# Performance work log

Hardware: AMD Instinct MI355X
Metric: run time of the kernel (lower is better)

## Reference

```python
import jax, jax.numpy as jnp
import numpy as np

DIM = 256
EPS = 1e-5

def setup_inputs() -> dict:
    key = jax.random.key(0)
    ks = jax.random.split(key, 10)
    B, S, D = 8, 4096, DIM
    sc = 1.0 / np.sqrt(D)
    return {
        "supervised_embedding": jax.random.normal(ks[0], (B, S, D), jnp.float32),
        "transformer_embedding": jax.random.normal(ks[1], (B, S, D), jnp.float32),
        "Wq": jax.random.normal(ks[2], (D, D), jnp.float32) * sc,
        "bq": jnp.zeros((D,), jnp.float32),
        "Wk": jax.random.normal(ks[3], (D, D), jnp.float32) * sc,
        "bk": jnp.zeros((D,), jnp.float32),
        "Wv": jax.random.normal(ks[4], (D, D), jnp.float32) * sc,
        "bv": jnp.zeros((D,), jnp.float32),
        "gamma": jnp.ones((D,), jnp.float32),
        "beta": jnp.zeros((D,), jnp.float32),
    }

def _layernorm(x, gamma, beta):
    mu = jnp.mean(x, axis=-1, keepdims=True)
    var = jnp.mean(jnp.square(x - mu), axis=-1, keepdims=True)
    return (x - mu) * jax.lax.rsqrt(var + EPS) * gamma + beta

def reference(supervised_embedding, transformer_embedding, Wq, bq, Wk, bk, Wv, bv, gamma, beta):
    # torch Linear: y = x @ W.T + b
    q = transformer_embedding @ Wq.T + bq          # [B,S,D]
    k = supervised_embedding @ Wk.T + bk           # [B,S,D]
    v = supervised_embedding @ Wv.T + bv           # [B,S,D]
    scale = 1.0 / jnp.sqrt(jnp.asarray(q.shape[-1], q.dtype))
    scores = jnp.einsum('bqd,bkd->bqk', q, k) * scale  # [B,S,S]
    w = jax.nn.softmax(scores, axis=-1)
    combined = jnp.einsum('bqk,bkd->bqd', w, v)    # [B,S,D]
    out = _layernorm(combined + transformer_embedding, gamma, beta)
    return jnp.squeeze(out, axis=1) if out.shape[1] == 1 else out
```

## Files before the change

kernel.cpp:

```cpp
#include <hip/hip_runtime.h>
#include <hip/hip_bf16.h>

typedef short s16x8 __attribute__((ext_vector_type(8)));
typedef unsigned short u16x4 __attribute__((ext_vector_type(4)));
typedef float f32x4 __attribute__((ext_vector_type(4)));
typedef unsigned short u16;

#define DEV static __device__ __forceinline__

#if __has_builtin(__builtin_amdgcn_exp2f)
#define EXP2F(x) __builtin_amdgcn_exp2f(x)
#else
#define EXP2F(x) exp2f(x)
#endif

constexpr int D    = 256;
constexpr int SEQ  = 4096;
constexpr int NB   = 8;
constexpr int NTOK = NB * SEQ;
constexpr size_t N_EMB = (size_t)NTOK * D;
constexpr size_t N_W   = (size_t)D * D;
constexpr float SM_C = 0.09016844005556021f;
constexpr float SMAX = 128.0f;

DEV u16 f2bf(float f){ unsigned v; __builtin_memcpy(&v,&f,4); v += 0x7fffu + ((v>>16)&1u); return (u16)(v>>16); }

DEV float rsum16(float v){
  v += __shfl_xor(v,1); v += __shfl_xor(v,2);
  v += __shfl_xor(v,4); v += __shfl_xor(v,8);
  return v;
}

DEV void gl2lds16(const u16* g, void* lds){
  __builtin_amdgcn_global_load_lds(
      (const __attribute__((address_space(1))) void*)g,
      (__attribute__((address_space(3))) void*)lds, 16, 0, 0);
}
DEV void lgkm_barrier(){
  __builtin_amdgcn_s_waitcnt(0xC07F);
  __builtin_amdgcn_s_barrier();
}

DEV s16x8 cvt8(const float* p){
  f32x4 u = *(const f32x4*)p;
  f32x4 w = *(const f32x4*)(p + 4);
  s16x8 t;
#pragma unroll
  for (int j = 0; j < 4; j++){ t[j] = (short)f2bf(u[j]); t[j+4] = (short)f2bf(w[j]); }
  return t;
}

__global__ __launch_bounds__(256)
void cvt_w(const float* __restrict__ Wq, const float* __restrict__ Wk,
           const float* __restrict__ Wv, u16* __restrict__ dst)
{
  size_t i = ((size_t)blockIdx.x*256 + threadIdx.x) * 4;
  const float* s = (i < N_W) ? (Wq + i) : (i < 2*N_W) ? (Wk + i - N_W) : (Wv + i - 2*N_W);
  f32x4 v = *(const f32x4*)s;
  u16x4 o;
#pragma unroll
  for (int j = 0; j < 4; j++) o[j] = f2bf(v[j]);
  *(u16x4*)(dst + i) = o;
}

__global__ __launch_bounds__(256, 2)
void qkv_proj(const float* __restrict__ TE, const float* __restrict__ SE,
              const u16* __restrict__ Wqb, const float* __restrict__ bq,
              const u16* __restrict__ Wkb, const float* __restrict__ bk,
              const u16* __restrict__ Wvb, const float* __restrict__ bv,
              u16* __restrict__ Qb, u16* __restrict__ Kb, u16* __restrict__ Vt)
{
  const int mode = blockIdx.y;
  const int t0   = blockIdx.x * 64;
  const int lane = threadIdx.x & 63;
  const int wv   = threadIdx.x >> 6;
  const int li   = lane & 15, grp = lane >> 4;

  const float* X    = (mode == 0) ? TE  : SE;
  const u16*   W    = (mode == 0) ? Wqb : (mode == 1) ? Wkb : Wvb;
  const float* bias = (mode == 0) ? bq  : (mode == 1) ? bk  : bv;

  if (mode < 2) {
    u16* Y = (mode == 0) ? Qb : Kb;
    const float* xrow = X + (size_t)(t0 + 16*wv + li) * D + grp*8;
    s16x8 a[8];
#pragma unroll
    for (int ks = 0; ks < 8; ks++) a[ks] = cvt8(xrow + ks*32);
    f32x4 acc[16];
#pragma unroll
    for (int i = 0; i < 16; i++) acc[i] = (f32x4){0.f,0.f,0.f,0.f};
#pragma unroll
    for (int nt = 0; nt < 16; nt++) {
      const u16* wrow = W + (size_t)(16*nt + li) * D + grp*8;
#pragma unroll
      for (int ks = 0; ks < 8; ks++) {
        s16x8 bf = *(const s16x8*)(wrow + ks*32);
        acc[nt] = __builtin_amdgcn_mfma_f32_16x16x32_bf16(a[ks], bf, acc[nt], 0,0,0);
      }
    }
#pragma unroll
    for (int nt = 0; nt < 16; nt++) {
      int col = li + 16*nt;
      float bb = bias[col];
#pragma unroll
      for (int r = 0; r < 4; r++) {
        int row = t0 + 16*wv + grp*4 + r;
        Y[(size_t)row*D + col] = f2bf(acc[nt][r] + bb);
      }
    }
  } else {
    f32x4 acc[16];
#pragma unroll
    for (int i = 0; i < 16; i++) acc[i] = (f32x4){0.f,0.f,0.f,0.f};
#pragma unroll
    for (int ks = 0; ks < 8; ks++) {
      s16x8 a[4], bb[4];
#pragma unroll
      for (int mt = 0; mt < 4; mt++)
        a[mt] = *(const s16x8*)(W + (size_t)(64*wv + 16*mt + li) * D + ks*32 + grp*8);
#pragma unroll
      for (int nt = 0; nt < 4; nt++)
        bb[nt] = cvt8(X + (size_t)(t0 + 16*nt + li) * D + ks*32 + grp*8);
#pragma unroll
      for (int mt = 0; mt < 4; mt++)
#pragma unroll
        for (int nt = 0; nt < 4; nt++)
          acc[mt*4+nt] = __builtin_amdgcn_mfma_f32_16x16x32_bf16(a[mt], bb[nt], acc[mt*4+nt], 0,0,0);
    }
    const int b = t0 >> 12, s0 = t0 & (SEQ - 1);
#pragma unroll
    for (int mt = 0; mt < 4; mt++) {
#pragma unroll
      for (int r = 0; r < 4; r++) {
        int o = 64*wv + 16*mt + grp*4 + r;
        float bb = bias[o];
        u16* yrow = Vt + ((size_t)b * D + o) * SEQ + s0;
#pragma unroll
        for (int nt = 0; nt < 4; nt++)
          yrow[16*nt + li] = f2bf(acc[mt*4+nt][r] + bb);
      }
    }
  }
}

constexpr int KB0   = 0;
constexpr int KB1   = 16384;
constexpr int P_OFF = 32768;
constexpr int PSTR  = 36;
constexpr int L_OFF = 37376;
constexpr int G_OFF = 37632;
constexpr int BE_OFF= 38656;
constexpr int LDS_SZ= 39680;
constexpr int NIT   = SEQ / 32;

__global__ __launch_bounds__(256, 2)
void attn_ln(const u16* __restrict__ Qb, const u16* __restrict__ Kb,
             const u16* __restrict__ Vt, const float* __restrict__ TE,
             const float* __restrict__ gamma, const float* __restrict__ beta,
             float* __restrict__ out)
{
  __shared__ __align__(16) char smem[LDS_SZ];
  const int tid  = threadIdx.x;
  const int lane = tid & 63, wv = tid >> 6;
  const int li   = lane & 15, grp = lane >> 4;
  const int b  = blockIdx.x & 7;
  const int q0 = (blockIdx.x >> 3) * 64;

  float* gam = (float*)(smem + G_OFF);
  float* bet = (float*)(smem + BE_OFF);
  gam[tid] = gamma[tid];
  bet[tid] = beta[tid];

  const u16* Kbase = Kb + (size_t)b * SEQ * D;
  const u16* Vbase = Vt + (size_t)b * D * SEQ;

  const u16* qrow = Qb + ((size_t)b*SEQ + q0 + 16*wv + li)*D + grp*8;
  s16x8 qf[8];
#pragma unroll
  for (int ks = 0; ks < 8; ks++) qf[ks] = *(const s16x8*)(qrow + ks*32);

  int soff[4];
#pragma unroll
  for (int c = 0; c < 4; c++) {
    int u = wv*4 + c;
    int r = 2*u + (lane >> 5);
    soff[c] = r*256 + (((lane & 31) ^ (r & 7)) * 8);
  }
  int voff[4];
#pragma unroll
  for (int nt = 0; nt < 4; nt++) voff[nt] = (64*wv + 16*nt + li)*SEQ + grp*8;

#pragma unroll
  for (int c = 0; c < 4; c++)
    gl2lds16(Kbase + soff[c], smem + KB0 + (wv*4 + c)*1024);

  f32x4 oacc[16];
#pragma unroll
  for (int i = 0; i < 16; i++) oacc[i] = (f32x4){0.f,0.f,0.f,0.f};
  float l_r[4] = {0.f,0.f,0.f,0.f};

  u16* Pl = (u16*)(smem + P_OFF);

  for (int it = 0; it < NIT; it++) {
    const int k0 = it * 32;
    __syncthreads();

    {
      const u16* Kt = Kbase + (size_t)((it+1 < NIT) ? (k0+32) : k0) * D;
      char* kbn = smem + ((it & 1) ? KB0 : KB1);
#pragma unroll
      for (int c = 0; c < 4; c++)
        gl2lds16(Kt + soff[c], kbn + (wv*4 + c)*1024);
    }
    s16x8 vf[4];
#pragma unroll
    for (int nt = 0; nt < 4; nt++)
      vf[nt] = *(const s16x8*)(Vbase + voff[nt] + k0);

    const char* kb = smem + ((it & 1) ? KB1 : KB0);
    f32x4 sa0 = {0.f,0.f,0.f,0.f}, sa1 = {0.f,0.f,0.f,0.f};
    {
      const int r0 = li, r1 = li + 16;
      const char* kp0 = kb + r0*512;
      const char* kp1 = kb + r1*512;
#pragma unroll
      for (int ks = 0; ks < 8; ks++) {
        s16x8 k0f = *(const s16x8*)(kp0 + 16*((4*ks + grp) ^ (r0 & 7)));
        sa0 = __builtin_amdgcn_mfma_f32_16x16x32_bf16(qf[ks], k0f, sa0, 0,0,0);
        s16x8 k1f = *(const s16x8*)(kp1 + 16*((4*ks + grp) ^ (r1 & 7)));
        sa1 = __builtin_amdgcn_mfma_f32_16x16x32_bf16(qf[ks], k1f, sa1, 0,0,0);
      }
    }

#pragma unroll
    for (int r = 0; r < 4; r++) {
      float p0 = EXP2F((sa0[r] - SMAX) * SM_C);
      float p1 = EXP2F((sa1[r] - SMAX) * SM_C);
      l_r[r] += p0 + p1;
      int row = 16*wv + grp*4 + r;
      Pl[row*PSTR + li]      = f2bf(p0);
      Pl[row*PSTR + li + 16] = f2bf(p1);
    }
    lgkm_barrier();

#pragma unroll
    for (int mt = 0; mt < 4; mt++) {
      s16x8 pf = *(const s16x8*)(smem + P_OFF + ((16*mt + li)*PSTR + grp*8)*2);
#pragma unroll
      for (int nt = 0; nt < 4; nt++)
        oacc[mt*4+nt] = __builtin_amdgcn_mfma_f32_16x16x32_bf16(pf, vf[nt], oacc[mt*4+nt], 0,0,0);
    }
  }

  float* l_lds = (float*)(smem + L_OFF);
  {
#pragma unroll
    for (int r = 0; r < 4; r++) {
      float lt = rsum16(l_r[r]);
      if (li == 0) l_lds[16*wv + grp*4 + r] = lt;
    }
  }
  __syncthreads();

  const float* Tg = TE + ((size_t)b*SEQ + q0) * D;
  float s1[4][4], s2[4][4];
#pragma unroll
  for (int mt = 0; mt < 4; mt++) {
#pragma unroll
    for (int r = 0; r < 4; r++) {
      int row = 16*mt + grp*4 + r;
      float linv = 1.0f / l_lds[row];
      float ps = 0.f, pq = 0.f;
#pragma unroll
      for (int nt = 0; nt < 4; nt++) {
        int d_ = 64*wv + 16*nt + li;
        float x = oacc[mt*4+nt][r] * linv + Tg[(size_t)row*D + d_];
        oacc[mt*4+nt][r] = x;
        ps += x; pq += x * x;
      }
      s1[mt][r] = rsum16(ps);
      s2[mt][r] = rsum16(pq);
    }
  }
  float* part1 = (float*)(smem + P_OFF);
  float* part2 = (float*)(smem + P_OFF + 1024);
  if (li == 0) {
#pragma unroll
    for (int mt = 0; mt < 4; mt++)
#pragma unroll
      for (int r = 0; r < 4; r++) {
        int row = 16*mt + grp*4 + r;
        part1[row*4 + wv] = s1[mt][r];
        part2[row*4 + wv] = s2[mt][r];
      }
  }
  __syncthreads();
#pragma unroll
  for (int mt = 0; mt < 4; mt++) {
#pragma unroll
    for (int r = 0; r < 4; r++) {
      int row = 16*mt + grp*4 + r;
      float su = part1[row*4+0] + part1[row*4+1] + part1[row*4+2] + part1[row*4+3];
      float sq = part2[row*4+0] + part2[row*4+1] + part2[row*4+2] + part2[row*4+3];
      float mu  = su * (1.0f/256.0f);
      float var = sq * (1.0f/256.0f) - mu*mu;
      float rstd = rsqrtf(var + 1e-5f);
      float* orow = out + ((size_t)b*SEQ + q0 + row) * D;
#pragma unroll
      for (int nt = 0; nt < 4; nt++) {
        int d_ = 64*wv + 16*nt + li;
        orow[d_] = (oacc[mt*4+nt][r] - mu) * rstd * gam[d_] + bet[d_];
      }
    }
  }
}

extern "C" void kernel_launch(void* const* d_in, const int* in_sizes, int n_in,
                              void* d_out, int out_size, void* d_ws, size_t ws_size,
                              hipStream_t stream)
{
  (void)in_sizes; (void)n_in; (void)out_size; (void)ws_size;
  const float* SE = (const float*)d_in[0];
  const float* TE = (const float*)d_in[1];
  const float* Wq = (const float*)d_in[2];
  const float* bq = (const float*)d_in[3];
  const float* Wk = (const float*)d_in[4];
  const float* bk = (const float*)d_in[5];
  const float* Wv = (const float*)d_in[6];
  const float* bv = (const float*)d_in[7];
  const float* gm = (const float*)d_in[8];
  const float* bt = (const float*)d_in[9];

  u16* Qb  = (u16*)d_ws;
  u16* Kb  = Qb + N_EMB;
  u16* Vtr = Kb + N_EMB;
  u16* Wqb = Vtr + N_EMB;
  u16* Wkb = Wqb + N_W;
  u16* Wvb = Wkb + N_W;

  cvt_w<<<dim3(3*N_W/1024), 256, 0, stream>>>(Wq, Wk, Wv, Wqb);
  qkv_proj<<<dim3(NTOK/64, 3), 256, 0, stream>>>(TE, SE, Wqb, bq, Wkb, bk, Wvb, bv, Qb, Kb, Vtr);
  attn_ln<<<dim3((SEQ/64) * NB), 256, 0, stream>>>(Qb, Kb, Vtr, TE, gm, bt, (float*)d_out);
}
```

Before: 368.2 us.

## Pre-convert embeddings to bf16 and tile QKV projection with LDS-resident weight strips

```diff
diff --git a/kernel.cpp b/kernel.cpp
--- a/kernel.cpp
+++ b/kernel.cpp
@@ -41,103 +41,124 @@
   __builtin_amdgcn_s_barrier();
 }
 
-DEV s16x8 cvt8(const float* p){
-  f32x4 u = *(const f32x4*)p;
-  f32x4 w = *(const f32x4*)(p + 4);
-  s16x8 t;
-#pragma unroll
-  for (int j = 0; j < 4; j++){ t[j] = (short)f2bf(u[j]); t[j+4] = (short)f2bf(w[j]); }
-  return t;
-}
-
 __global__ __launch_bounds__(256)
-void cvt_w(const float* __restrict__ Wq, const float* __restrict__ Wk,
-           const float* __restrict__ Wv, u16* __restrict__ dst)
+void cvt_all(const float* __restrict__ TE, const float* __restrict__ SE,
+             const float* __restrict__ Wq, const float* __restrict__ Wk,
+             const float* __restrict__ Wv, u16* __restrict__ dst)
 {
-  size_t i = ((size_t)blockIdx.x*256 + threadIdx.x) * 4;
-  const float* s = (i < N_W) ? (Wq + i) : (i < 2*N_W) ? (Wk + i - N_W) : (Wv + i - 2*N_W);
-  f32x4 v = *(const f32x4*)s;
-  u16x4 o;
-#pragma unroll
-  for (int j = 0; j < 4; j++) o[j] = f2bf(v[j]);
-  *(u16x4*)(dst + i) = o;
-}
-
-__global__ __launch_bounds__(256, 2)
-void qkv_proj(const float* __restrict__ TE, const float* __restrict__ SE,
+  const size_t total4 = (2*N_EMB + 3*N_W) / 4;
+  for (size_t i = (size_t)blockIdx.x*256 + threadIdx.x; i < total4;
+       i += (size_t)gridDim.x*256) {
+    size_t e = i*4;
+    const float* s;
+    if      (e < N_EMB)            s = TE + e;
+    else if (e < 2*N_EMB)          s = SE + (e - N_EMB);
+    else if (e < 2*N_EMB + N_W)    s = Wq + (e - 2*N_EMB);
+    else if (e < 2*N_EMB + 2*N_W)  s = Wk + (e - 2*N_EMB - N_W);
+    else                           s = Wv + (e - 2*N_EMB - 2*N_W);
+    f32x4 v = *(const f32x4*)s;
+    u16x4 o;
+#pragma unroll
+    for (int j = 0; j < 4; j++) o[j] = f2bf(v[j]);
+    *(u16x4*)(dst + e) = o;
+  }
+}
+
+__global__ __launch_bounds__(256, 3)
+void qkv_proj(const u16* __restrict__ TEb, const u16* __restrict__ SEb,
               const u16* __restrict__ Wqb, const float* __restrict__ bq,
               const u16* __restrict__ Wkb, const float* __restrict__ bk,
               const u16* __restrict__ Wvb, const float* __restrict__ bv,
               u16* __restrict__ Qb, u16* __restrict__ Kb, u16* __restrict__ Vt)
 {
-  const int mode = blockIdx.y;
-  const int t0   = blockIdx.x * 64;
-  const int lane = threadIdx.x & 63;
-  const int wv   = threadIdx.x >> 6;
+  __shared__ __align__(16) char wlds[32768];
+  const int tid  = threadIdx.x;
+  const int lane = tid & 63, wv = tid >> 6;
   const int li   = lane & 15, grp = lane >> 4;
-
-  const float* X    = (mode == 0) ? TE  : SE;
+  const int mode  = blockIdx.y >> 2;
+  const int strip = blockIdx.y & 3;
+  const int o0    = strip * 64;
+  const int tbase = blockIdx.x * 512;
+
+  const u16*   X    = (mode == 0) ? TEb : SEb;
   const u16*   W    = (mode == 0) ? Wqb : (mode == 1) ? Wkb : Wvb;
   const float* bias = (mode == 0) ? bq  : (mode == 1) ? bk  : bv;
 
-  if (mode < 2) {
-    u16* Y = (mode == 0) ? Qb : Kb;
-    const float* xrow = X + (size_t)(t0 + 16*wv + li) * D + grp*8;
-    s16x8 a[8];
-#pragma unroll
-    for (int ks = 0; ks < 8; ks++) a[ks] = cvt8(xrow + ks*32);
+#pragma unroll
+  for (int c = 0; c < 8; c++) {
+    int g = tid + 256*c;
+    int r = g >> 5, jj = g & 31;
+    *(s16x8*)(wlds + r*512 + 16*(jj ^ (r & 7))) =
+        *(const s16x8*)(W + (size_t)(o0 + r)*D + jj*8);
+  }
+  __syncthreads();
+
+#pragma unroll 1
+  for (int tt = 0; tt < 2; tt++) {
+    const int base = tbase + tt*256 + wv*64;
     f32x4 acc[16];
 #pragma unroll
     for (int i = 0; i < 16; i++) acc[i] = (f32x4){0.f,0.f,0.f,0.f};
-#pragma unroll
-    for (int nt = 0; nt < 16; nt++) {
-      const u16* wrow = W + (size_t)(16*nt + li) * D + grp*8;
+
+    if (mode < 2) {
 #pragma unroll
       for (int ks = 0; ks < 8; ks++) {
-        s16x8 bf = *(const s16x8*)(wrow + ks*32);
-        acc[nt] = __builtin_amdgcn_mfma_f32_16x16x32_bf16(a[ks], bf, acc[nt], 0,0,0);
-      }
-    }
-#pragma unroll
-    for (int nt = 0; nt < 16; nt++) {
-      int col = li + 16*nt;
-      float bb = bias[col];
-#pragma unroll
-      for (int r = 0; r < 4; r++) {
-        int row = t0 + 16*wv + grp*4 + r;
-        Y[(size_t)row*D + col] = f2bf(acc[nt][r] + bb);
-      }
-    }
-  } else {
-    f32x4 acc[16];
-#pragma unroll
-    for (int i = 0; i < 16; i++) acc[i] = (f32x4){0.f,0.f,0.f,0.f};
-#pragma unroll
-    for (int ks = 0; ks < 8; ks++) {
-      s16x8 a[4], bb[4];
-#pragma unroll
-      for (int mt = 0; mt < 4; mt++)
-        a[mt] = *(const s16x8*)(W + (size_t)(64*wv + 16*mt + li) * D + ks*32 + grp*8);
-#pragma unroll
-      for (int nt = 0; nt < 4; nt++)
-        bb[nt] = cvt8(X + (size_t)(t0 + 16*nt + li) * D + ks*32 + grp*8);
-#pragma unroll
-      for (int mt = 0; mt < 4; mt++)
-#pragma unroll
-        for (int nt = 0; nt < 4; nt++)
-          acc[mt*4+nt] = __builtin_amdgcn_mfma_f32_16x16x32_bf16(a[mt], bb[nt], acc[mt*4+nt], 0,0,0);
-    }
-    const int b = t0 >> 12, s0 = t0 & (SEQ - 1);
-#pragma unroll
-    for (int mt = 0; mt < 4; mt++) {
-#pragma unroll
-      for (int r = 0; r < 4; r++) {
-        int o = 64*wv + 16*mt + grp*4 + r;
-        float bb = bias[o];
-        u16* yrow = Vt + ((size_t)b * D + o) * SEQ + s0;
-#pragma unroll
-        for (int nt = 0; nt < 4; nt++)
-          yrow[16*nt + li] = f2bf(acc[mt*4+nt][r] + bb);
+        s16x8 a[4], bw[4];
+#pragma unroll
+        for (int mt = 0; mt < 4; mt++)
+          a[mt] = *(const s16x8*)(X + (size_t)(base + 16*mt + li)*D + ks*32 + grp*8);
+#pragma unroll
+        for (int nt = 0; nt < 4; nt++) {
+          int r = 16*nt + li;
+          bw[nt] = *(const s16x8*)(wlds + r*512 + 16*((4*ks + grp) ^ (r & 7)));
+        }
+#pragma unroll
+        for (int mt = 0; mt < 4; mt++)
+#pragma unroll
+          for (int nt = 0; nt < 4; nt++)
+            acc[mt*4+nt] = __builtin_amdgcn_mfma_f32_16x16x32_bf16(a[mt], bw[nt], acc[mt*4+nt], 0,0,0);
+      }
+      u16* Y = (mode == 0) ? Qb : Kb;
+#pragma unroll
+      for (int nt = 0; nt < 4; nt++) {
+        int col = o0 + 16*nt + li;
+        float bb = bias[col];
+#pragma unroll
+        for (int mt = 0; mt < 4; mt++)
+#pragma unroll
+          for (int r = 0; r < 4; r++)
+            Y[(size_t)(base + 16*mt + grp*4 + r)*D + col] = f2bf(acc[mt*4+nt][r] + bb);
+      }
+    } else {
+#pragma unroll
+      for (int ks = 0; ks < 8; ks++) {
+        s16x8 aw[4], bx[4];
+#pragma unroll
+        for (int at = 0; at < 4; at++) {
+          int r = 16*at + li;
+          aw[at] = *(const s16x8*)(wlds + r*512 + 16*((4*ks + grp) ^ (r & 7)));
+        }
+#pragma unroll
+        for (int bt = 0; bt < 4; bt++)
+          bx[bt] = *(const s16x8*)(X + (size_t)(base + 16*bt + li)*D + ks*32 + grp*8);
+#pragma unroll
+        for (int at = 0; at < 4; at++)
+#pragma unroll
+          for (int bt = 0; bt < 4; bt++)
+            acc[at*4+bt] = __builtin_amdgcn_mfma_f32_16x16x32_bf16(aw[at], bx[bt], acc[at*4+bt], 0,0,0);
+      }
+      const int b = base >> 12, s0 = base & (SEQ - 1);
+#pragma unroll
+      for (int at = 0; at < 4; at++) {
+#pragma unroll
+        for (int r = 0; r < 4; r++) {
+          int o = o0 + 16*at + grp*4 + r;
+          float bb = bias[o];
+          u16* yrow = Vt + ((size_t)b*D + o)*SEQ + s0;
+#pragma unroll
+          for (int bt = 0; bt < 4; bt++)
+            yrow[16*bt + li] = f2bf(acc[at*4+bt][r] + bb);
+        }
       }
     }
   }
@@ -153,7 +174,7 @@
 constexpr int LDS_SZ= 39680;
 constexpr int NIT   = SEQ / 32;
 
-__global__ __launch_bounds__(256, 2)
+__global__ __launch_bounds__(256, 3)
 void attn_ln(const u16* __restrict__ Qb, const u16* __restrict__ Kb,
              const u16* __restrict__ Vt, const float* __restrict__ TE,
              const float* __restrict__ gamma, const float* __restrict__ beta,
@@ -334,11 +355,14 @@
   u16* Qb  = (u16*)d_ws;
   u16* Kb  = Qb + N_EMB;
   u16* Vtr = Kb + N_EMB;
-  u16* Wqb = Vtr + N_EMB;
+  u16* CVT = Vtr + N_EMB;
+  u16* TEb = CVT;
+  u16* SEb = TEb + N_EMB;
+  u16* Wqb = SEb + N_EMB;
   u16* Wkb = Wqb + N_W;
   u16* Wvb = Wkb + N_W;
 
-  cvt_w<<<dim3(3*N_W/1024), 256, 0, stream>>>(Wq, Wk, Wv, Wqb);
-  qkv_proj<<<dim3(NTOK/64, 3), 256, 0, stream>>>(TE, SE, Wqb, bq, Wkb, bk, Wvb, bv, Qb, Kb, Vtr);
+  cvt_all<<<2048, 256, 0, stream>>>(TE, SE, Wq, Wk, Wv, CVT);
+  qkv_proj<<<dim3(NTOK/512, 12), 256, 0, stream>>>(TEb, SEb, Wqb, bq, Wkb, bk, Wvb, bv, Qb, Kb, Vtr);
   attn_ln<<<dim3((SEQ/64) * NB), 256, 0, stream>>>(Qb, Kb, Vtr, TE, gm, bt, (float*)d_out);
 }
```

Measured after the change: 340.1 us. 1.08x faster.
